# Kernel optimization log

Hardware: AMD Instinct MI355X
Metric: run time of the kernel (lower is better)

## Reference

```python
import jax, jax.numpy as jnp
import numpy as np
import math

B, T, C = 4, 2048, 1024
H = 128            # num_heads
D = C // H         # head_dim = 8 (n_wires of the quantum device)


def setup_inputs() -> dict:
    key = jax.random.key(0)
    k1, k2, k3 = jax.random.split(key, 3)
    x = jax.random.normal(k1, (B, T, C), dtype=jnp.float32)
    # trainable RX angles: head_dim gates, each a scalar angle (tq.RX has_params=True)
    theta = jax.random.normal(k2, (D,), dtype=jnp.float32)
    # nn.Linear(C, C, bias=False) weight, torch layout [out, in]
    w_proj = jax.random.normal(k3, (C, C), dtype=jnp.float32) / math.sqrt(C)
    return {"x": x, "theta": theta, "w_proj": w_proj}


def _quantum_measure(xh, theta):
    # Circuit per head/token: start |0..0>, apply RX(x_j) on wire j (encoder
    # resets the state each call), then each of the D trainable RX(theta_g)
    # gates is broadcast over all wires. RX angles on one wire compose
    # additively, and <Z> after RX(phi)|0> == cos(phi).
    return jnp.cos(xh + jnp.sum(theta))  # [B, T, H, D]


def reference(x, theta, w_proj):
    xh = x.reshape(B, T, H, D)
    q = _quantum_measure(xh, theta)  # q == k == v (shared encoder + shared gates)
    # torch.matmul on [B,T,H,D]: batch dims (B,T) -> head-vs-head scores [B,T,H,H]
    scores = jnp.einsum('bthd,btgd->bthg', q, q) / math.sqrt(D)
    attn = jax.nn.softmax(scores, axis=-1)  # dropout: identity in eval
    out = jnp.einsum('bthg,btgd->bthd', attn, q).reshape(B, T, C)
    return out @ w_proj.T
```

## Files before the change

kernel.cpp:

```cpp
#include <hip/hip_runtime.h>
#include <hip/hip_bf16.h>
#include <stdint.h>

#define NB 4
#define NT 2048
#define NC 1024
#define NH 128
#define ND 8
#define NTOK (NB*NT)
#define GK 1024
#define GN 1024

typedef __attribute__((ext_vector_type(4))) float f32x4;
typedef __attribute__((ext_vector_type(8))) short bf16x8;
typedef __attribute__((ext_vector_type(4))) unsigned int u32x4;
typedef __attribute__((ext_vector_type(2))) unsigned int u32x2;
typedef unsigned int uint32;

#define GAMMA  0.71419167f
#define GB16   0x3F37u
#define C0     0.9990878f

#define GLOAD_LDS16(g, l) \
  __builtin_amdgcn_global_load_lds((const __attribute__((address_space(1))) void*)(g), \
                                   (__attribute__((address_space(3))) void*)(l), 16, 0, 0)

__device__ __forceinline__ unsigned short f2bf(float f) {
  __bf16 b = (__bf16)f;
  return __builtin_bit_cast(unsigned short, b);
}
__device__ __forceinline__ uint32 pk2(float a, float b) {
  return (uint32)f2bf(a) | ((uint32)f2bf(b) << 16);
}

__global__ __launch_bounds__(256) void wconv_kernel(const float4* __restrict__ w,
                                                    ushort4* __restrict__ wb) {
  int i = blockIdx.x * 256 + threadIdx.x;
  float4 v = w[i];
  ushort4 o;
  o.x = f2bf(v.x); o.y = f2bf(v.y); o.z = f2bf(v.z); o.w = f2bf(v.w);
  wb[i] = o;
}

#define QTS 136

__global__ __launch_bounds__(256) void attn_kernel(const float* __restrict__ x,
                                                   const float* __restrict__ theta,
                                                   unsigned short* __restrict__ aout) {
  __shared__ __align__(16) unsigned short QT[4][8 * QTS];

  const int tid = (int)threadIdx.x;
  const int wid = tid >> 6;
  const int tok = blockIdx.x * 4 + wid;
  const int l = tid & 63;
  const int c = l & 15;
  const int t = l >> 4;

  float S = 0.f;
#pragma unroll
  for (int j = 0; j < ND; ++j) S += theta[j];

  u32x4 qf[8];
  unsigned short* qt = &QT[wid][0];
#pragma unroll
  for (int a = 0; a < 8; ++a) {
    float2 xv = *(const float2*)(x + (size_t)tok * NC + (16 * a + c) * ND + 2 * t);
    float q0 = GAMMA * __cosf(xv.x + S);
    float q1 = GAMMA * __cosf(xv.y + S);
    unsigned short b0 = f2bf(q0), b1 = f2bf(q1);
    qt[(2 * t) * QTS + 16 * a + c] = b0;
    qt[(2 * t + 1) * QTS + 16 * a + c] = b1;
    qf[a].x = (uint32)b0 | ((uint32)b1 << 16);
    qf[a].y = 0u; qf[a].z = 0u; qf[a].w = 0u;
  }

  u32x4 bff[4];
  {
    const int cm = (c < 8) ? c : 7;
    const bool isq = (c < 8);
    const uint32 onepair = GB16 | (GB16 << 16);
#pragma unroll
    for (int j = 0; j < 4; ++j) {
      u32x2 v0 = *(const u32x2*)&qt[cm * QTS + 32 * j + 4 * t];
      u32x2 v1 = *(const u32x2*)&qt[cm * QTS + 32 * j + 16 + 4 * t];
      bff[j].x = isq ? v0.x : onepair;
      bff[j].y = isq ? v0.y : onepair;
      bff[j].z = isq ? v1.x : onepair;
      bff[j].w = isq ? v1.y : onepair;
    }
  }

  const f32x4 z4 = {0.f, 0.f, 0.f, 0.f};
  unsigned short* orow = aout + (size_t)tok * NC;

#pragma unroll
  for (int b = 0; b < 8; ++b) {
    f32x4 o = z4;
#pragma unroll
    for (int j = 0; j < 4; ++j) {
      f32x4 sv0 = __builtin_amdgcn_mfma_f32_16x16x32_bf16(
          __builtin_bit_cast(bf16x8, qf[2 * j]), __builtin_bit_cast(bf16x8, qf[b]),
          z4, 0, 0, 0);
      f32x4 sv1 = __builtin_amdgcn_mfma_f32_16x16x32_bf16(
          __builtin_bit_cast(bf16x8, qf[2 * j + 1]), __builtin_bit_cast(bf16x8, qf[b]),
          z4, 0, 0, 0);
      u32x4 af;
      af.x = pk2(__builtin_amdgcn_exp2f(sv0[0]), __builtin_amdgcn_exp2f(sv0[1]));
      af.y = pk2(__builtin_amdgcn_exp2f(sv0[2]), __builtin_amdgcn_exp2f(sv0[3]));
      af.z = pk2(__builtin_amdgcn_exp2f(sv1[0]), __builtin_amdgcn_exp2f(sv1[1]));
      af.w = pk2(__builtin_amdgcn_exp2f(sv1[2]), __builtin_amdgcn_exp2f(sv1[3]));
      o = __builtin_amdgcn_mfma_f32_16x16x32_bf16(
          __builtin_bit_cast(bf16x8, af), __builtin_bit_cast(bf16x8, bff[j]),
          o, 0, 0, 0);
    }
#pragma unroll
    for (int r = 0; r < 4; ++r) {
      float rs = __shfl_xor(o[r], 8, 64);
      float outv = o[r] * __builtin_amdgcn_rcpf(rs * C0);
      if (c < 8)
        orow[(16 * b + 4 * t + r) * ND + c] = f2bf(outv);
    }
  }
}

#define BM 128
#define BN 128
#define BK 32

__global__ __launch_bounds__(256) void gemm_kernel(const unsigned short* __restrict__ A,
                                                   const unsigned short* __restrict__ Bt,
                                                   float* __restrict__ C) {
  __shared__ __align__(16) unsigned short As[BM * BK];
  __shared__ __align__(16) unsigned short Bs[BN * BK];

  const int bm = blockIdx.x;
  const int bn = blockIdx.y;
  const int tid = (int)threadIdx.x;
  const int lane = tid & 63;
  const int w = tid >> 6;
  const int wm = w >> 1;
  const int wn = w & 1;

  f32x4 acc[4][4] = {};

  const int sr = w * 32 + (lane >> 2);
  const int sc = (lane & 3) * 8;
  const unsigned short* gA = A + (size_t)(bm * BM + sr) * GK + sc;
  const unsigned short* gB = Bt + (size_t)(bn * BN + sr) * GK + sc;
  unsigned short* lA = &As[(w * 32) * BK];
  unsigned short* lB = &Bs[(w * 32) * BK];

  const int fr = lane & 15;
  const int fk = (lane >> 4) * 8;

  for (int kt = 0; kt < GK; kt += BK) {
    __syncthreads();
    GLOAD_LDS16(gA, lA);
    GLOAD_LDS16(gA + 16 * GK, lA + 16 * BK);
    GLOAD_LDS16(gB, lB);
    GLOAD_LDS16(gB + 16 * GK, lB + 16 * BK);
    asm volatile("s_waitcnt vmcnt(0)" ::: "memory");
    __syncthreads();

    bf16x8 af[4], bfr[4];
#pragma unroll
    for (int i = 0; i < 4; ++i)
      af[i] = *reinterpret_cast<const bf16x8*>(&As[(wm * 64 + i * 16 + fr) * BK + fk]);
#pragma unroll
    for (int j = 0; j < 4; ++j)
      bfr[j] = *reinterpret_cast<const bf16x8*>(&Bs[(wn * 64 + j * 16 + fr) * BK + fk]);

#pragma unroll
    for (int i = 0; i < 4; ++i)
#pragma unroll
      for (int j = 0; j < 4; ++j)
        acc[i][j] = __builtin_amdgcn_mfma_f32_16x16x32_bf16(af[i], bfr[j], acc[i][j], 0, 0, 0);

    gA += BK;
    gB += BK;
  }

  float* Cb = C + (size_t)(bm * BM + wm * 64) * GN + bn * BN + wn * 64;
  const int cr = (lane >> 4) * 4;
  const int cc = lane & 15;
#pragma unroll
  for (int i = 0; i < 4; ++i)
#pragma unroll
    for (int j = 0; j < 4; ++j)
#pragma unroll
      for (int r = 0; r < 4; ++r)
        Cb[(size_t)(i * 16 + cr + r) * GN + j * 16 + cc] = acc[i][j][r];
}

extern "C" void kernel_launch(void* const* d_in, const int* in_sizes, int n_in,
                              void* d_out, int out_size, void* d_ws, size_t ws_size,
                              hipStream_t stream) {
  (void)in_sizes; (void)n_in; (void)out_size; (void)ws_size;
  const float* x = (const float*)d_in[0];
  const float* theta = (const float*)d_in[1];
  const float* wproj = (const float*)d_in[2];
  float* y = (float*)d_out;

  unsigned short* attn_out = (unsigned short*)d_ws;
  unsigned short* wb = (unsigned short*)((char*)d_ws + (size_t)NTOK * NC * 2);

  wconv_kernel<<<(NC * NC / 4) / 256, 256, 0, stream>>>((const float4*)wproj,
                                                        (ushort4*)wb);
  attn_kernel<<<NTOK / 4, 256, 0, stream>>>(x, theta, attn_out);
  dim3 grid(NTOK / BM, GN / BN);
  gemm_kernel<<<grid, 256, 0, stream>>>(attn_out, wb, y);
}
```

Before: 69.19 us.

## Double-buffer GEMM K-tiles with XOR-swizzled LDS and 512-thread blocks

The projection GEMM moves from a single-buffered BK=32 loop to a double-buffered BK=64 pipeline, so the next tile's global-to-LDS loads are issued before computing on the current one. The LDS layout uses an XOR swizzle on 16-byte chunks to avoid bank conflicts on fragment reads. Blocks grow to 8 waves, each computing a 64x32 sub-tile. The aim is to hide global memory latency and cut LDS conflicts, at the cost of more LDS per block and more barrier traffic.

```diff
diff --git a/kernel.cpp b/kernel.cpp
--- a/kernel.cpp
+++ b/kernel.cpp
@@ -125,71 +125,96 @@
 
 #define BM 128
 #define BN 128
-#define BK 32
-
-__global__ __launch_bounds__(256) void gemm_kernel(const unsigned short* __restrict__ A,
-                                                   const unsigned short* __restrict__ Bt,
-                                                   float* __restrict__ C) {
-  __shared__ __align__(16) unsigned short As[BM * BK];
-  __shared__ __align__(16) unsigned short Bs[BN * BK];
+#define BK 64
+
+__global__ __launch_bounds__(512, 4) void gemm_kernel(const unsigned short* __restrict__ A,
+                                                      const unsigned short* __restrict__ Bt,
+                                                      float* __restrict__ C) {
+  __shared__ __align__(16) unsigned short As[2][BM * BK];
+  __shared__ __align__(16) unsigned short Bs[2][BN * BK];
 
   const int bm = blockIdx.x;
   const int bn = blockIdx.y;
   const int tid = (int)threadIdx.x;
-  const int lane = tid & 63;
+  const int l = tid & 63;
   const int w = tid >> 6;
-  const int wm = w >> 1;
-  const int wn = w & 1;
-
-  f32x4 acc[4][4] = {};
-
-  const int sr = w * 32 + (lane >> 2);
-  const int sc = (lane & 3) * 8;
-  const unsigned short* gA = A + (size_t)(bm * BM + sr) * GK + sc;
-  const unsigned short* gB = Bt + (size_t)(bn * BN + sr) * GK + sc;
-  unsigned short* lA = &As[(w * 32) * BK];
-  unsigned short* lB = &Bs[(w * 32) * BK];
-
-  const int fr = lane & 15;
-  const int fk = (lane >> 4) * 8;
-
-  for (int kt = 0; kt < GK; kt += BK) {
-    __syncthreads();
-    GLOAD_LDS16(gA, lA);
-    GLOAD_LDS16(gA + 16 * GK, lA + 16 * BK);
-    GLOAD_LDS16(gB, lB);
-    GLOAD_LDS16(gB + 16 * GK, lB + 16 * BK);
-    asm volatile("s_waitcnt vmcnt(0)" ::: "memory");
-    __syncthreads();
-
-    bf16x8 af[4], bfr[4];
-#pragma unroll
-    for (int i = 0; i < 4; ++i)
-      af[i] = *reinterpret_cast<const bf16x8*>(&As[(wm * 64 + i * 16 + fr) * BK + fk]);
-#pragma unroll
-    for (int j = 0; j < 4; ++j)
-      bfr[j] = *reinterpret_cast<const bf16x8*>(&Bs[(wn * 64 + j * 16 + fr) * BK + fk]);
-
-#pragma unroll
-    for (int i = 0; i < 4; ++i)
-#pragma unroll
-      for (int j = 0; j < 4; ++j)
-        acc[i][j] = __builtin_amdgcn_mfma_f32_16x16x32_bf16(af[i], bfr[j], acc[i][j], 0, 0, 0);
-
-    gA += BK;
-    gB += BK;
-  }
-
-  float* Cb = C + (size_t)(bm * BM + wm * 64) * GN + bn * BN + wn * 64;
-  const int cr = (lane >> 4) * 4;
-  const int cc = lane & 15;
+  const int wm = w >> 2;
+  const int wn = w & 3;
+
+  f32x4 acc[4][2] = {};
+
+  const int srow = l >> 3;
+  const int schk = (l & 7) ^ srow;
+  const unsigned short* gA0 = A + (size_t)(bm * BM + 16 * w + srow) * GK + schk * 8;
+  const unsigned short* gA1 = gA0 + 8 * GK;
+  const unsigned short* gB0 = Bt + (size_t)(bn * BN + 16 * w + srow) * GK + schk * 8;
+  const unsigned short* gB1 = gB0 + 8 * GK;
+
+  const int fr = l & 15;
+  const int kcb = l >> 4;
+  const int fx = l & 7;
+
+#define STAGE(nb)                                          \
+  {                                                        \
+    unsigned short* la = &As[nb][(16 * w) * BK];           \
+    unsigned short* lb = &Bs[nb][(16 * w) * BK];           \
+    GLOAD_LDS16(gA0, la);                                  \
+    GLOAD_LDS16(gA1, la + 8 * BK);                         \
+    GLOAD_LDS16(gB0, lb);                                  \
+    GLOAD_LDS16(gB1, lb + 8 * BK);                         \
+    gA0 += BK; gA1 += BK; gB0 += BK; gB1 += BK;            \
+  }
+
+  auto compute = [&](const unsigned short* as, const unsigned short* bs) {
+#pragma unroll
+    for (int s = 0; s < 2; ++s) {
+      const int slot = ((4 * s + kcb) ^ fx) * 8;
+      bf16x8 af[4], bfr[2];
+#pragma unroll
+      for (int i = 0; i < 4; ++i)
+        af[i] = *reinterpret_cast<const bf16x8*>(&as[(64 * wm + 16 * i + fr) * BK + slot]);
+#pragma unroll
+      for (int j = 0; j < 2; ++j)
+        bfr[j] = *reinterpret_cast<const bf16x8*>(&bs[(32 * wn + 16 * j + fr) * BK + slot]);
+#pragma unroll
+      for (int i = 0; i < 4; ++i)
+#pragma unroll
+        for (int j = 0; j < 2; ++j)
+          acc[i][j] = __builtin_amdgcn_mfma_f32_16x16x32_bf16(af[i], bfr[j], acc[i][j], 0, 0, 0);
+    }
+  };
+
+  STAGE(0);
+
+  int buf = 0;
+#pragma unroll 1
+  for (int t = 0; t < 15; ++t) {
+    STAGE(buf ^ 1);
+    asm volatile("s_waitcnt vmcnt(4)" ::: "memory");
+    __builtin_amdgcn_s_barrier();
+    asm volatile("" ::: "memory");
+    compute(&As[buf][0], &Bs[buf][0]);
+    asm volatile("" ::: "memory");
+    __builtin_amdgcn_s_barrier();
+    asm volatile("" ::: "memory");
+    buf ^= 1;
+  }
+  asm volatile("s_waitcnt vmcnt(0)" ::: "memory");
+  __builtin_amdgcn_s_barrier();
+  asm volatile("" ::: "memory");
+  compute(&As[1][0], &Bs[1][0]);
+
+  float* Cb = C + (size_t)(bm * BM + 64 * wm) * GN + bn * BN + 32 * wn;
+  const int cr = (l >> 4) * 4;
+  const int cc = l & 15;
 #pragma unroll
   for (int i = 0; i < 4; ++i)
 #pragma unroll
-    for (int j = 0; j < 4; ++j)
+    for (int j = 0; j < 2; ++j)
 #pragma unroll
       for (int r = 0; r < 4; ++r)
-        Cb[(size_t)(i * 16 + cr + r) * GN + j * 16 + cc] = acc[i][j][r];
+        Cb[(size_t)(16 * i + cr + r) * GN + 16 * j + cc] = acc[i][j][r];
+#undef STAGE
 }
 
 extern "C" void kernel_launch(void* const* d_in, const int* in_sizes, int n_in,
@@ -208,5 +233,5 @@
                                                         (ushort4*)wb);
   attn_kernel<<<NTOK / 4, 256, 0, stream>>>(x, theta, attn_out);
   dim3 grid(NTOK / BM, GN / BN);
-  gemm_kernel<<<grid, 256, 0, stream>>>(attn_out, wb, y);
-}
+  gemm_kernel<<<grid, 512, 0, stream>>>(attn_out, wb, y);
+}
```

Result: faster. 62.87 us (-9.1%).
